# Kernel tuning notes

Hardware: AMD Instinct MI355X
Metric: run time of the kernel (lower is better)

The kernel has to match this reference:

```python
import jax, jax.numpy as jnp
import numpy as np

N = 8192      # nodes
DIN = 128     # in_channels
DH = 64       # hidden_channels (dim_out, num_heads=1)
DOUT = 32     # out_channels
RATIO = 0.5
K_KEEP = int(np.ceil(RATIO * N))  # SAGPooling keep count (single graph)
LN_EPS = 1e-5


def _linear_params(k, fan_in, fan_out):
    kw, kb = jax.random.split(k)
    W = jax.random.normal(kw, (fan_in, fan_out), dtype=jnp.float32) / jnp.sqrt(jnp.float32(fan_in))
    b = jax.random.normal(kb, (fan_out,), dtype=jnp.float32) * 0.01
    return W, b


def setup_inputs() -> dict:
    key = jax.random.key(0)
    ks = jax.random.split(key, 8)
    x = jax.random.normal(ks[0], (N, DIN), dtype=jnp.float32)
    batch = jnp.zeros((N,), dtype=jnp.int64)  # single graph
    Wq, bq = _linear_params(ks[1], DIN, DH)
    Wk, bk = _linear_params(ks[2], DIN, DH)
    Wv, bv = _linear_params(ks[3], DIN, DH)
    gcn_W, gcn_b = _linear_params(ks[4], DH, DH)       # GCNConv weight/bias
    score_W, score_b = _linear_params(ks[5], DH, 1)    # SAGPooling score GCNConv
    ln_g = jnp.ones((DH,), dtype=jnp.float32)
    ln_b = jnp.zeros((DH,), dtype=jnp.float32)
    head_W, head_b = _linear_params(ks[6], DH, DOUT)
    return dict(x=x, batch=batch, Wq=Wq, bq=bq, Wk=Wk, bk=bk, Wv=Wv, bv=bv,
                gcn_W=gcn_W, gcn_b=gcn_b, score_W=score_W, score_b=score_b,
                ln_g=ln_g, ln_b=ln_b, head_W=head_W, head_b=head_b)


def _forward(x, Wq, bq, Wk, bk, Wv, bv, gcn_W, gcn_b, score_W, score_b,
             ln_g, ln_b, head_W, head_b):
    # --- self-attention over all nodes (num_heads = 1) ---
    Q = x @ Wq + bq                                        # [N, DH]
    K = x @ Wk + bk
    V = x @ Wv + bv
    attn = jax.nn.softmax(Q @ K.T / jnp.sqrt(jnp.float32(DH)), axis=-1)  # [N, N]
    h = attn @ V                                           # [N, DH]

    # --- edge construction: threshold attention, ensure self-loops ---
    # (attn > 0.5).nonzero() -> edge set; empty -> self-loop fallback; then
    # add_self_loops. Dense equivalent: A = max(mask, I).
    eye = jnp.eye(N, dtype=x.dtype)
    A = jnp.maximum((attn > 0.5).astype(x.dtype), eye)     # [N, N], diag = 1

    # symmetric GCN normalization  D^{-1/2} A D^{-1/2}
    dinv = jax.lax.rsqrt(A.sum(axis=1))                    # [N]
    An = dinv[:, None] * A * dinv[None, :]                 # [N, N]

    # --- GCNConv layer ---
    g = An @ (h @ gcn_W) + gcn_b                           # [N, DH]

    # --- SAGPooling: GCNConv scorer -> tanh -> global top-k (single graph) ---
    score = jnp.tanh((An @ (g @ score_W) + score_b).squeeze(-1))  # [N]
    top_scores, perm = jax.lax.top_k(score, K_KEEP)        # sorted desc, like PyG topk
    xp = g[perm] * top_scores[:, None]                     # [K, DH], multiplier = 1

    # --- LayerNorm + ReLU (dropout is identity in eval) ---
    mu = xp.mean(axis=-1, keepdims=True)
    var = xp.var(axis=-1, keepdims=True)
    xp = (xp - mu) * jax.lax.rsqrt(var + LN_EPS) * ln_g + ln_b
    xp = jax.nn.relu(xp)

    # --- prediction head ---
    return xp @ head_W + head_b                            # [K, DOUT]


def reference(x, batch, Wq, bq, Wk, bk, Wv, bv, gcn_W, gcn_b,
              score_W, score_b, ln_g, ln_b, head_W, head_b):
    del batch  # single graph; grouping has no effect on the math
    return _forward(x, Wq, bq, Wk, bk, Wv, bv, gcn_W, gcn_b,
                    score_W, score_b, ln_g, ln_b, head_W, head_b)
```

## Files before the change

### kernel.cpp

```cpp
#include <hip/hip_runtime.h>
#include <hip/hip_bf16.h>
#include <cstdio>

typedef __hip_bfloat16 bf16;
typedef __attribute__((ext_vector_type(8))) short v8s;
typedef __attribute__((ext_vector_type(4))) short v4s;
typedef __attribute__((ext_vector_type(4))) float v4f;
typedef __attribute__((ext_vector_type(4))) double v4d;

#define MFMA16(a, b, c) __builtin_amdgcn_mfma_f32_16x16x32_bf16((a), (b), (c), 0, 0, 0)

#define NN 8192
#define DIN 128
#define DH 64
#define DOUT 32
#define KKEEP 4096
#define SPLITS 8
#define SPATT 8

__device__ __forceinline__ float bf2f(bf16 v) { return __bfloat162float(v); }
__device__ __forceinline__ short f2bfs(float f) {
  __hip_bfloat16 h = __float2bfloat16(f);
  return *reinterpret_cast<short*>(&h);
}
__device__ __forceinline__ bf16 f2bf(float v) { return __float2bfloat16(v); }

__device__ __forceinline__ double exp_d(double s) {
  const double L2E    = 1.4426950408889634074;
  const double LN2_HI = 6.93147180369123816490e-01;
  const double LN2_LO = 1.90821492927058770002e-10;
  double t  = s * L2E;
  double kf = rint(t);
  double r  = fma(-kf, LN2_HI, s);
  r = fma(-kf, LN2_LO, r);
  double p = 1.0 / 362880.0;
  p = fma(p, r, 1.0 / 40320.0);
  p = fma(p, r, 1.0 / 5040.0);
  p = fma(p, r, 1.0 / 720.0);
  p = fma(p, r, 1.0 / 120.0);
  p = fma(p, r, 1.0 / 24.0);
  p = fma(p, r, 1.0 / 6.0);
  p = fma(p, r, 0.5);
  p = fma(p, r, 1.0);
  p = fma(p, r, 1.0);
  int k = (int)kf;
  long long bits = ((long long)(1023 + k)) << 52;
  double sc = __longlong_as_double(bits);
  return p * sc;
}

__global__ void k0_ucb(const float* __restrict__ gW, const float* __restrict__ sW,
                       const float* __restrict__ gb, double* __restrict__ u) {
  int c = threadIdx.x;
  double acc = 0.0, accb = 0.0;
  for (int d = 0; d < DH; ++d) {
    double swd = (double)sW[d];
    acc  = fma((double)gW[c * DH + d], swd, acc);
    accb = fma((double)gb[d], swd, accb);
  }
  u[c] = acc;
  if (c == 0) u[64] = accb;
}

__global__ __launch_bounds__(256) void k1_prep(
    const float* __restrict__ x, const float* __restrict__ Wq, const float* __restrict__ bq,
    const float* __restrict__ Wk, const float* __restrict__ bk, const float* __restrict__ Wv,
    const float* __restrict__ bv, const double* __restrict__ u,
    double* __restrict__ Qd, double* __restrict__ Kd, double* __restrict__ w,
    bf16* __restrict__ Qb, bf16* __restrict__ Kb, bf16* __restrict__ Vt) {
  __shared__ double xs[16][DIN];
  int t = threadIdx.x;
  int nb = blockIdx.x * 16;
  for (int idx = t; idx < 16 * DIN; idx += 256)
    xs[idx >> 7][idx & 127] = (double)x[(size_t)nb * DIN + idx];
  __syncthreads();
  int d = t & 63;
  int sub = t >> 6;
  double bqd = (double)bq[d];
  double bkd = (double)bk[d];
  double bvd = (double)bv[d];
  double ud = u[d];
  for (int pass = 0; pass < 4; ++pass) {
    int n = pass * 4 + sub;
    double aq = bqd, ak = bkd, av = bvd;
#pragma unroll 8
    for (int c = 0; c < DIN; ++c) {
      double xv = xs[n][c];
      aq = fma(xv, (double)Wq[c * DH + d], aq);
      ak = fma(xv, (double)Wk[c * DH + d], ak);
      av = fma(xv, (double)Wv[c * DH + d], av);
    }
    aq *= 0.125;
    int node = nb + n;
    Qd[(size_t)node * DH + d] = aq;
    Kd[(size_t)node * DH + d] = ak;
    Qb[(size_t)node * DH + d] = f2bf((float)aq);
    Kb[(size_t)node * DH + d] = f2bf((float)ak);
    Vt[(size_t)d * NN + node] = f2bf((float)av);
    double pw = av * ud;
#pragma unroll
    for (int off = 32; off; off >>= 1) pw += __shfl_xor(pw, off);
    if (d == 0) w[node] = pw;
  }
}

__global__ __launch_bounds__(256) void k2_scores(
    const double* __restrict__ Qd, const double* __restrict__ Kd, const double* __restrict__ w,
    double* __restrict__ Zp, double* __restrict__ Wp, double* __restrict__ Ep, int* __restrict__ Jp) {
  __shared__ __align__(16) double Kbuf[2][32][66];
  const int t = threadIdx.x;
  const int wv = t >> 6;
  const int l = t & 63;
  const int li = l & 15, lg = l >> 4;
  const int rb = (blockIdx.x & 127) * 64;
  const int sp = blockIdx.x >> 7;
  const int cbeg = sp * (NN / SPLITS);

  double qreg[16];
  const double* qrow = Qd + (size_t)(rb + 16 * wv + li) * DH + lg;
#pragma unroll
  for (int tt = 0; tt < 16; ++tt) qreg[tt] = qrow[4 * tt];

  const int r0 = t >> 5, c20 = (t & 31) * 2;

  {
    const double* src = Kd + (size_t)cbeg * DH;
#pragma unroll
    for (int k = 0; k < 4; ++k) {
      int r = r0 + 8 * k;
      *(double2*)&Kbuf[0][r][c20] = *(const double2*)&src[r * DH + c20];
    }
  }
  __syncthreads();

  double Zt[4] = {0, 0, 0, 0}, Wt[4] = {0, 0, 0, 0}, Et[4] = {-1, -1, -1, -1};
  int Jt[4] = {0, 0, 0, 0};

  const int NT = (NN / SPLITS) / 32;
  for (int kt = 0; kt < NT; ++kt) {
    const int buf = kt & 1;
    const bool pf = (kt + 1 < NT);
    double2 st[4];
    if (pf) {
      const double* src = Kd + (size_t)(cbeg + (kt + 1) * 32) * DH;
#pragma unroll
      for (int k = 0; k < 4; ++k) st[k] = *(const double2*)&src[(r0 + 8 * k) * DH + c20];
    }
#pragma unroll
    for (int hf = 0; hf < 2; ++hf) {
      v4d a0 = (v4d){0.0, 0.0, 0.0, 0.0};
      v4d a1 = (v4d){0.0, 0.0, 0.0, 0.0};
#pragma unroll
      for (int tt = 0; tt < 8; ++tt) {
        double b0 = Kbuf[buf][li + 16 * hf][4 * tt + lg];
        double b1 = Kbuf[buf][li + 16 * hf][4 * (tt + 8) + lg];
        a0 = __builtin_amdgcn_mfma_f64_16x16x4f64(qreg[tt], b0, a0, 0, 0, 0);
        a1 = __builtin_amdgcn_mfma_f64_16x16x4f64(qreg[tt + 8], b1, a1, 0, 0, 0);
      }
      const int col = cbeg + kt * 32 + 16 * hf + li;
      const double wj = w[col];
#pragma unroll
      for (int v = 0; v < 4; ++v) {
        double e = exp_d(a0[v] + a1[v]);
        Zt[v] += e;
        Wt[v] = fma(e, wj, Wt[v]);
        if (e > Et[v]) { Et[v] = e; Jt[v] = col; }
      }
    }
    if (pf) {
#pragma unroll
      for (int k = 0; k < 4; ++k) *(double2*)&Kbuf[buf ^ 1][r0 + 8 * k][c20] = st[k];
    }
    __syncthreads();
  }

#pragma unroll
  for (int v = 0; v < 4; ++v) {
#pragma unroll
    for (int m = 1; m < 16; m <<= 1) {
      Zt[v] += __shfl_xor(Zt[v], m);
      Wt[v] += __shfl_xor(Wt[v], m);
      double e2 = __shfl_xor(Et[v], m);
      int j2 = __shfl_xor(Jt[v], m);
      if (e2 > Et[v] || (e2 == Et[v] && j2 < Jt[v])) { Et[v] = e2; Jt[v] = j2; }
    }
  }
  if (li == 0) {
#pragma unroll
    for (int v = 0; v < 4; ++v) {
      int row = rb + 16 * wv + lg + 4 * v;
      Zp[sp * NN + row] = Zt[v];
      Wp[sp * NN + row] = Wt[v];
      Ep[sp * NN + row] = Et[v];
      Jp[sp * NN + row] = Jt[v];
    }
  }
}

__global__ void k3_combine(const double* __restrict__ Zp, const double* __restrict__ Wp,
                           const double* __restrict__ Ep, const int* __restrict__ Jp,
                           double* __restrict__ tau, int* __restrict__ extra, int* __restrict__ jmA) {
  int i = blockIdx.x * 256 + threadIdx.x;
  double Z = 0, W = 0, E = -1;
  int J = 0;
  for (int sp = 0; sp < SPLITS; ++sp) {
    Z += Zp[sp * NN + i];
    W += Wp[sp * NN + i];
    double e = Ep[sp * NN + i];
    if (e > E || (e == E && Jp[sp * NN + i] < J)) { E = e; J = Jp[sp * NN + i]; }
  }
  tau[i] = W / Z;
  extra[i] = (E > 0.5 * Z) && (J != i);
  jmA[i] = J & (NN - 1);
}

__global__ __launch_bounds__(256) void k4_mfma(const bf16* __restrict__ Qb, const bf16* __restrict__ Kb,
                                               const bf16* __restrict__ Vt,
                                               float* __restrict__ hp, float* __restrict__ zp) {
  __shared__ __align__(16) short P[4][16 * 40];
  const int t = threadIdx.x;
  const int wv = t >> 6;
  const int l = t & 63, g = l >> 4, li = l & 15;
  const int qb = (blockIdx.x & 127) * 64 + wv * 16;
  const int sp = blockIdx.x >> 7;
  short* Pw = &P[wv][0];
  const v8s q0 = *(const v8s*)(Qb + (size_t)(qb + li) * DH + g * 8);
  const v8s q1 = *(const v8s*)(Qb + (size_t)(qb + li) * DH + 32 + g * 8);
  v4f hacc[4];
#pragma unroll
  for (int db = 0; db < 4; ++db) hacc[db] = (v4f){0.f, 0.f, 0.f, 0.f};
  float zl = 0.f;
  const int kbeg = sp * (NN / SPATT);
  for (int jb = kbeg; jb < kbeg + NN / SPATT; jb += 32) {
    const bf16* kp = Kb + (size_t)(jb + li) * DH + g * 8;
    v8s ka0 = *(const v8s*)(kp);
    v8s ka1 = *(const v8s*)(kp + 32);
    v8s kb0 = *(const v8s*)(kp + 16 * DH);
    v8s kb1 = *(const v8s*)(kp + 16 * DH + 32);
    v4f c0 = (v4f){0.f, 0.f, 0.f, 0.f}, c1 = (v4f){0.f, 0.f, 0.f, 0.f};
    c0 = MFMA16(ka0, q0, c0);
    c0 = MFMA16(ka1, q1, c0);
    c1 = MFMA16(kb0, q0, c1);
    c1 = MFMA16(kb1, q1, c1);
    v4s p0, p1;
#pragma unroll
    for (int r = 0; r < 4; ++r) {
      short b0 = f2bfs(__expf(c0[r]));
      short b1 = f2bfs(__expf(c1[r]));
      p0[r] = b0;
      p1[r] = b1;
      zl += bf2f(*reinterpret_cast<bf16*>(&b0));
      zl += bf2f(*reinterpret_cast<bf16*>(&b1));
    }
    *(v4s*)&Pw[li * 40 + g * 4] = p0;
    *(v4s*)&Pw[li * 40 + 16 + g * 4] = p1;
    __syncthreads();
    v8s pf = *(const v8s*)&Pw[li * 40 + g * 8];
#pragma unroll
    for (int db = 0; db < 4; ++db) {
      const v8s vb = *(const v8s*)(Vt + (size_t)(db * 16 + li) * NN + jb + g * 8);
      hacc[db] = MFMA16(pf, vb, hacc[db]);
    }
    __syncthreads();
  }
  zl += __shfl_xor(zl, 16);
  zl += __shfl_xor(zl, 32);
  if (g == 0) zp[sp * NN + qb + li] = zl;
#pragma unroll
  for (int r = 0; r < 4; ++r) {
    int row = qb + g * 4 + r;
#pragma unroll
    for (int db = 0; db < 4; ++db)
      hp[((size_t)sp * NN + row) * DH + db * 16 + li] = hacc[db][r];
  }
}

__global__ __launch_bounds__(256) void k9_hM(const float* __restrict__ hp, const float* __restrict__ zp,
                                             const float* __restrict__ gW, float* __restrict__ M) {
  __shared__ float xs[4][DH];
  int t = threadIdx.x;
  int sub = t >> 6, d = t & 63;
  int n = blockIdx.x * 4 + sub;
  float Z = 0.f, H = 0.f;
#pragma unroll
  for (int sp = 0; sp < SPATT; ++sp) {
    Z += zp[sp * NN + n];
    H += hp[((size_t)sp * NN + n) * DH + d];
  }
  xs[sub][d] = H / Z;
  __syncthreads();
  float acc = 0.f;
#pragma unroll 8
  for (int c = 0; c < DH; ++c) acc = fmaf(xs[sub][c], gW[c * DH + d], acc);
  M[(size_t)n * DH + d] = acc;
}

__global__ void k5_t(const double* __restrict__ tau, const int* __restrict__ extra,
                     const int* __restrict__ jmA, const double* __restrict__ u, double* __restrict__ tarr) {
  int i = blockIdx.x * 256 + threadIdx.x;
  int ex = extra[i];
  double di = ex ? 0.70710678118654752440 : 1.0;
  double acc = di * tau[i];
  if (ex) {
    int j = jmA[i] & (NN - 1);
    double dj = extra[j] ? 0.70710678118654752440 : 1.0;
    acc = fma(dj, tau[j], acc);
  }
  tarr[i] = fma(di, acc, u[64]);
}

__global__ void k6_pre(const double* __restrict__ tarr, const int* __restrict__ extra,
                       const int* __restrict__ jmA, const float* __restrict__ score_b,
                       double* __restrict__ pre, float* __restrict__ sc32, int* __restrict__ cnt) {
  int i = blockIdx.x * 256 + threadIdx.x;
  int ex = extra[i];
  double di = ex ? 0.70710678118654752440 : 1.0;
  double acc = di * tarr[i];
  if (ex) {
    int j = jmA[i] & (NN - 1);
    double dj = extra[j] ? 0.70710678118654752440 : 1.0;
    acc = fma(dj, tarr[j], acc);
  }
  double p = fma(di, acc, (double)score_b[0]);
  pre[i] = p;
  sc32[i] = (float)tanh(p);
  cnt[i] = 0;
}

__global__ void k7_rank(const double* __restrict__ pre, int* __restrict__ cnt) {
  int i = (blockIdx.x & 31) * 256 + threadIdx.x;
  int j0 = (blockIdx.x >> 5) * 512;
  double si = pre[i];
  int c = 0;
#pragma unroll 4
  for (int j = j0; j < j0 + 512; j += 2) {
    double2 pj = *(const double2*)(pre + j);
    c += (pj.x > si || (pj.x == si && j < i));
    c += (pj.y > si || (pj.y == si && (j + 1) < i));
  }
  atomicAdd(&cnt[i], c);
}

__global__ void k8_sel(const int* __restrict__ cnt, int* __restrict__ sel) {
  int i = blockIdx.x * 256 + threadIdx.x;
  unsigned r = (unsigned)cnt[i];
  if (r < KKEEP) sel[r] = i;
}

__global__ __launch_bounds__(256) void k11_head(const float* __restrict__ M, const int* __restrict__ extra,
                                                const int* __restrict__ jmA, const float* __restrict__ gb,
                                                const float* __restrict__ sc32, const int* __restrict__ sel,
                                                const float* __restrict__ lg, const float* __restrict__ lb,
                                                const float* __restrict__ hW, const float* __restrict__ hb,
                                                float* __restrict__ out) {
  __shared__ float xs[4][DH];
  int t = threadIdx.x;
  int wv = t >> 6, d = t & 63;
  int p = blockIdx.x * 4 + wv;
  int i = sel[p] & (NN - 1);
  int ex = extra[i];
  float di = ex ? 0.70710678f : 1.0f;
  float acc0 = di * M[(size_t)i * DH + d];
  if (ex) {
    int j = jmA[i] & (NN - 1);
    acc0 = fmaf(extra[j] ? 0.70710678f : 1.0f, M[(size_t)j * DH + d], acc0);
  }
  float gval = fmaf(di, acc0, gb[d]);
  float v = gval * sc32[i];
  float s1 = v;
#pragma unroll
  for (int off = 32; off; off >>= 1) s1 += __shfl_xor(s1, off);
  float mu = s1 * (1.0f / 64.0f);
  float dv = v - mu;
  float s2 = dv * dv;
#pragma unroll
  for (int off = 32; off; off >>= 1) s2 += __shfl_xor(s2, off);
  float var = s2 * (1.0f / 64.0f);
  float xn = dv * rsqrtf(var + 1e-5f) * lg[d] + lb[d];
  xs[wv][d] = fmaxf(xn, 0.0f);
  __syncthreads();
  if (t < 128) {
    int r = t >> 5, o = t & 31;
    float acc = hb[o];
#pragma unroll 8
    for (int c = 0; c < DH; ++c) acc = fmaf(xs[r][c], hW[c * DOUT + o], acc);
    out[(size_t)(blockIdx.x * 4 + r) * DOUT + o] = acc;
  }
}

#define MB 1048576ull
constexpr size_t OFF_QD   = 0 * MB;
constexpr size_t OFF_KD   = 4 * MB;
constexpr size_t OFF_M    = 16 * MB;
constexpr size_t OFF_ZP   = 20 * MB;
constexpr size_t OFF_WP   = 21 * MB;
constexpr size_t OFF_EP   = 22 * MB;
constexpr size_t OFF_JP   = 23 * MB;
constexpr size_t OFF_W    = 24 * MB;
constexpr size_t OFF_U    = 25 * MB;
constexpr size_t OFF_TAU  = 26 * MB;
constexpr size_t OFF_EX   = 27 * MB;
constexpr size_t OFF_JM   = 28 * MB;
constexpr size_t OFF_T    = 29 * MB;
constexpr size_t OFF_PRE  = 30 * MB;
constexpr size_t OFF_SC   = 31 * MB;
constexpr size_t OFF_CNT  = 32 * MB;
constexpr size_t OFF_SEL  = 33 * MB;
constexpr size_t OFF_HP   = 34 * MB;
constexpr size_t OFF_ZATT = 50 * MB;
constexpr size_t OFF_QB   = 51 * MB;
constexpr size_t OFF_KB   = 52 * MB;
constexpr size_t OFF_VT   = 53 * MB;
constexpr size_t WS_NEEDED = 54 * MB;

extern "C" void kernel_launch(void* const* d_in, const int* in_sizes, int n_in,
                              void* d_out, int out_size, void* d_ws, size_t ws_size,
                              hipStream_t stream) {
  if (n_in < 16 || ws_size < WS_NEEDED || out_size != KKEEP * DOUT) {
    fprintf(stderr, "[sag] GUARD ws=%zu need=%zu n_in=%d out=%d\n", ws_size, WS_NEEDED, n_in, out_size);
    return;
  }
  const float* x   = (const float*)d_in[0];
  const float* Wq  = (const float*)d_in[2];
  const float* bq  = (const float*)d_in[3];
  const float* Wk  = (const float*)d_in[4];
  const float* bk  = (const float*)d_in[5];
  const float* Wv  = (const float*)d_in[6];
  const float* bv  = (const float*)d_in[7];
  const float* gW  = (const float*)d_in[8];
  const float* gb  = (const float*)d_in[9];
  const float* sW  = (const float*)d_in[10];
  const float* sb  = (const float*)d_in[11];
  const float* lg  = (const float*)d_in[12];
  const float* lb  = (const float*)d_in[13];
  const float* hW  = (const float*)d_in[14];
  const float* hb  = (const float*)d_in[15];
  float* out = (float*)d_out;

  char* ws = (char*)d_ws;
  double* Qd  = (double*)(ws + OFF_QD);
  double* Kd  = (double*)(ws + OFF_KD);
  bf16*   Qb  = (bf16*)(ws + OFF_QB);
  bf16*   Kb  = (bf16*)(ws + OFF_KB);
  bf16*   Vt  = (bf16*)(ws + OFF_VT);
  float*  M   = (float*)(ws + OFF_M);
  double* Zp  = (double*)(ws + OFF_ZP);
  double* Wp  = (double*)(ws + OFF_WP);
  double* Ep  = (double*)(ws + OFF_EP);
  int*    Jp  = (int*)(ws + OFF_JP);
  double* w   = (double*)(ws + OFF_W);
  double* u   = (double*)(ws + OFF_U);
  double* tau = (double*)(ws + OFF_TAU);
  int*    ex  = (int*)(ws + OFF_EX);
  int*    jm  = (int*)(ws + OFF_JM);
  double* tarr= (double*)(ws + OFF_T);
  double* pre = (double*)(ws + OFF_PRE);
  float*  sc32= (float*)(ws + OFF_SC);
  int*    cnt = (int*)(ws + OFF_CNT);
  int*    sel = (int*)(ws + OFF_SEL);
  float*  hp  = (float*)(ws + OFF_HP);
  float*  zatt= (float*)(ws + OFF_ZATT);

  hipLaunchKernelGGL(k0_ucb, dim3(1), dim3(64), 0, stream, gW, sW, gb, u);
  hipLaunchKernelGGL(k1_prep, dim3(512), dim3(256), 0, stream, x, Wq, bq, Wk, bk, Wv, bv, u,
                     Qd, Kd, w, Qb, Kb, Vt);
  hipLaunchKernelGGL(k2_scores, dim3(128 * SPLITS), dim3(256), 0, stream, Qd, Kd, w, Zp, Wp, Ep, Jp);
  hipLaunchKernelGGL(k3_combine, dim3(32), dim3(256), 0, stream, Zp, Wp, Ep, Jp, tau, ex, jm);
  hipLaunchKernelGGL(k4_mfma, dim3(128 * SPATT), dim3(256), 0, stream, Qb, Kb, Vt, hp, zatt);
  hipLaunchKernelGGL(k9_hM, dim3(2048), dim3(256), 0, stream, hp, zatt, gW, M);
  hipLaunchKernelGGL(k5_t, dim3(32), dim3(256), 0, stream, tau, ex, jm, u, tarr);
  hipLaunchKernelGGL(k6_pre, dim3(32), dim3(256), 0, stream, tarr, ex, jm, sb, pre, sc32, cnt);
  hipLaunchKernelGGL(k7_rank, dim3(512), dim3(256), 0, stream, pre, cnt);
  hipLaunchKernelGGL(k8_sel, dim3(32), dim3(256), 0, stream, cnt, sel);
  hipLaunchKernelGGL(k11_head, dim3(1024), dim3(256), 0, stream, M, ex, jm, gb, sc32, sel,
                     lg, lb, hW, hb, out);
}
```

Before: 404.9 us.

## Software-pipeline exp epilogue behind next tile's MFMA and rotate K-tile start per block

The score kernel now computes the MFMA dot products for tile p while applying exp, the running sums and the argmax update to the scores of tile p-1, so the FP64 exp work can overlap the matrix ops. Each block also starts its walk over K tiles at a block-dependent rotation, spreading concurrent reads of the same K rows across the column split. The argmax tie-break now prefers the smaller column index, which keeps results independent of visit order. Keeping the previous tile's scores live adds eight double registers per thread, which may affect occupancy.

```diff
diff --git a/kernel.cpp b/kernel.cpp
--- a/kernel.cpp
+++ b/kernel.cpp
@@ -115,6 +115,8 @@
   const int rb = (blockIdx.x & 127) * 64;
   const int sp = blockIdx.x >> 7;
   const int cbeg = sp * (NN / SPLITS);
+  const int NT = (NN / SPLITS) / 32;
+  const int rot = blockIdx.x & (NT - 1);
 
   double qreg[16];
   const double* qrow = Qd + (size_t)(rb + 16 * wv + li) * DH + lg;
@@ -124,7 +126,7 @@
   const int r0 = t >> 5, c20 = (t & 31) * 2;
 
   {
-    const double* src = Kd + (size_t)cbeg * DH;
+    const double* src = Kd + (size_t)(cbeg + rot * 32) * DH;
 #pragma unroll
     for (int k = 0; k < 4; ++k) {
       int r = r0 + 8 * k;
@@ -135,17 +137,21 @@
 
   double Zt[4] = {0, 0, 0, 0}, Wt[4] = {0, 0, 0, 0}, Et[4] = {-1, -1, -1, -1};
   int Jt[4] = {0, 0, 0, 0};
-
-  const int NT = (NN / SPLITS) / 32;
-  for (int kt = 0; kt < NT; ++kt) {
-    const int buf = kt & 1;
-    const bool pf = (kt + 1 < NT);
+  double sPrev[8];
+  int pcb = 0;
+
+  for (int p = 0; p < NT; ++p) {
+    const int kt = (rot + p) & (NT - 1);
+    const int buf = p & 1;
+    const bool pf = (p + 1 < NT);
     double2 st[4];
     if (pf) {
-      const double* src = Kd + (size_t)(cbeg + (kt + 1) * 32) * DH;
+      const int ktn = (rot + p + 1) & (NT - 1);
+      const double* src = Kd + (size_t)(cbeg + ktn * 32) * DH;
 #pragma unroll
       for (int k = 0; k < 4; ++k) st[k] = *(const double2*)&src[(r0 + 8 * k) * DH + c20];
     }
+    double sNew[8];
 #pragma unroll
     for (int hf = 0; hf < 2; ++hf) {
       v4d a0 = (v4d){0.0, 0.0, 0.0, 0.0};
@@ -157,14 +163,21 @@
         a0 = __builtin_amdgcn_mfma_f64_16x16x4f64(qreg[tt], b0, a0, 0, 0, 0);
         a1 = __builtin_amdgcn_mfma_f64_16x16x4f64(qreg[tt + 8], b1, a1, 0, 0, 0);
       }
-      const int col = cbeg + kt * 32 + 16 * hf + li;
-      const double wj = w[col];
-#pragma unroll
-      for (int v = 0; v < 4; ++v) {
-        double e = exp_d(a0[v] + a1[v]);
-        Zt[v] += e;
-        Wt[v] = fma(e, wj, Wt[v]);
-        if (e > Et[v]) { Et[v] = e; Jt[v] = col; }
+#pragma unroll
+      for (int v = 0; v < 4; ++v) sNew[hf * 4 + v] = a0[v] + a1[v];
+    }
+    if (p > 0) {
+#pragma unroll
+      for (int hf = 0; hf < 2; ++hf) {
+        const int col = pcb + 16 * hf + li;
+        const double wj = w[col];
+#pragma unroll
+        for (int v = 0; v < 4; ++v) {
+          double e = exp_d(sPrev[hf * 4 + v]);
+          Zt[v] += e;
+          Wt[v] = fma(e, wj, Wt[v]);
+          if (e > Et[v] || (e == Et[v] && col < Jt[v])) { Et[v] = e; Jt[v] = col; }
+        }
       }
     }
     if (pf) {
@@ -172,6 +185,21 @@
       for (int k = 0; k < 4; ++k) *(double2*)&Kbuf[buf ^ 1][r0 + 8 * k][c20] = st[k];
     }
     __syncthreads();
+#pragma unroll
+    for (int s = 0; s < 8; ++s) sPrev[s] = sNew[s];
+    pcb = cbeg + kt * 32;
+  }
+#pragma unroll
+  for (int hf = 0; hf < 2; ++hf) {
+    const int col = pcb + 16 * hf + li;
+    const double wj = w[col];
+#pragma unroll
+    for (int v = 0; v < 4; ++v) {
+      double e = exp_d(sPrev[hf * 4 + v]);
+      Zt[v] += e;
+      Wt[v] = fma(e, wj, Wt[v]);
+      if (e > Et[v] || (e == Et[v] && col < Jt[v])) { Et[v] = e; Jt[v] = col; }
+    }
   }
 
 #pragma unroll
```

Result: slower. 458.0 us (+13.1%).
